# Optimization experiments

Hardware: AMD Instinct MI355X
Metric: run time of the kernel (lower is better)

## Reference

```python
import jax, jax.numpy as jnp
import numpy as np

B, N, F_IN, F_OUT = 16, 2048, 512, 512


def setup_inputs() -> dict:
    key = jax.random.key(0)
    k1, k2, k3 = jax.random.split(key, 3)
    x = jax.random.normal(k1, (B, N, F_IN), dtype=jnp.float32)
    adj = jax.random.uniform(k2, (N, N), dtype=jnp.float32)
    # Kaiming uniform fan_out: bound = sqrt(6 / fan_out)
    bound = np.sqrt(6.0 / F_OUT)
    weight = jax.random.uniform(k3, (F_IN, F_OUT), dtype=jnp.float32,
                                minval=-bound, maxval=bound)
    bias = jnp.zeros((F_OUT,), dtype=jnp.float32)
    return {"x": x, "adj": adj, "weight": weight, "bias": bias}


def reference(x, adj, weight, bias):
    # Symmetric degree normalization: D^{-1/2} A D^{-1/2}
    deg = adj.sum(axis=1)                                   # [N]
    deg_inv_sqrt = jnp.where(deg > 0, jax.lax.rsqrt(deg), 0.0)
    # row/column rescale instead of diag matmuls (same math, O(N^2))
    norm_adj = adj * deg_inv_sqrt[:, None] * deg_inv_sqrt[None, :]
    support = jnp.einsum('bni,io->bno', x, weight)          # [B,N,F_OUT]
    output = jnp.einsum('nm,bmo->bno', norm_adj, support)   # [B,N,F_OUT]
    return output + bias
```

## Files before the change

kernel.cpp:

```cpp
#include <hip/hip_runtime.h>
#include <hip/hip_bf16.h>
#include <stdint.h>

typedef __attribute__((ext_vector_type(8))) __bf16 bf16x8;
typedef __attribute__((ext_vector_type(4))) float f32x4;
typedef unsigned short u16;

__device__ __forceinline__ u16 f2bf(float f) {
  unsigned u = __builtin_bit_cast(unsigned, f);
  unsigned r = 0x7FFFu + ((u >> 16) & 1u);
  return (u16)((u + r) >> 16);
}

__device__ __forceinline__ u16 f2bf_hw(float f) {
  __hip_bfloat16 h = __float2bfloat16(f);
  return __builtin_bit_cast(u16, h);
}

__device__ __forceinline__ void gload16(const void* g, void* l) {
  __builtin_amdgcn_global_load_lds(
      (__attribute__((address_space(1))) void*)(g),
      (__attribute__((address_space(3))) void*)(l),
      16, 0, 0);
}

__global__ void row_deg_k(const float* __restrict__ adj, float* __restrict__ dis, int N) {
  int row = blockIdx.x;
  const float4* a = (const float4*)(adj + (size_t)row * N);
  float s = 0.f;
  for (int j = threadIdx.x; j < N / 4; j += 256) {
    float4 v = a[j];
    s += v.x + v.y + v.z + v.w;
  }
#pragma unroll
  for (int off = 32; off > 0; off >>= 1) s += __shfl_down(s, off, 64);
  __shared__ float wsum[4];
  if ((threadIdx.x & 63) == 0) wsum[threadIdx.x >> 6] = s;
  __syncthreads();
  if (threadIdx.x == 0) {
    float t = wsum[0] + wsum[1] + wsum[2] + wsum[3];
    dis[row] = (t > 0.f) ? (1.0f / sqrtf(t)) : 0.f;
  }
}

__global__ void conv_wt_k(const float* __restrict__ w, u16* __restrict__ wt) {
  int idx = blockIdx.x * 256 + threadIdx.x;
  int i = idx >> 9, o = idx & 511;
  wt[o * 512 + i] = f2bf(w[idx]);
}

__global__ void make_nadj_k(const float* __restrict__ adj, const float* __restrict__ dis,
                            u16* __restrict__ o, int N) {
  int idx = blockIdx.x * 256 + threadIdx.x;
  int i = idx >> 9;
  int j4 = (idx & 511) * 4;
  float di = dis[i];
  float4 a = ((const float4*)adj)[idx];
  ushort4 u;
  u.x = f2bf(a.x * di * dis[j4 + 0]);
  u.y = f2bf(a.y * di * dis[j4 + 1]);
  u.z = f2bf(a.z * di * dis[j4 + 2]);
  u.w = f2bf(a.w * di * dis[j4 + 3]);
  ((ushort4*)o)[idx] = u;
}

__launch_bounds__(512, 2)
__global__ void gemm1_xw_k(const float* __restrict__ X,
                           const u16* __restrict__ Wt,
                           u16* __restrict__ Ct, int M) {
  __shared__ __align__(16) u16 lds[65536];

  const int tid = threadIdx.x;
  const int lane = tid & 63;
  const int wid = tid >> 6;
  const int wr = wid >> 2;
  const int wc = wid & 3;

  const int flat = blockIdx.x;
  const int wg = (flat & 7) * 32 + (flat >> 3);
  const int m_t = wg >> 1;
  const int n_t = wg & 1;
  const int rowBase = m_t * 256;
  const int colBase = n_t * 256;

  const int lr = tid >> 3;
  const int kkl = (tid & 7) * 8;
  const int s = (lr & 7) << 3;
  const int kswz = kkl ^ s;
  const float* gX = X + (size_t)(rowBase + lr) * 512 + kkl;
  const u16* gB = Wt + (size_t)(colBase + lr) * 512 + kswz;
  u16* lAsw = lds + lr * 64 + kswz;
  u16* lB = lds + 32768 + lr * 64 + kkl;

  const int fr = lane & 15;
  const int rswz = (lane & 7) << 3;
  const int kp0 = ((lane >> 4) * 8) ^ rswz;
  const int kp1 = (32 | ((lane >> 4) * 8)) ^ rswz;
  const u16* fA = lds + (wr * 128 + fr) * 64;
  const u16* fB = lds + 32768 + (wc * 64 + fr) * 64;

  f32x4 acc[8][4] = {};
  f32x4 xv[4][2];

  const int NT = 8;

#define LOADX(t)                                                                     \
  _Pragma("unroll") for (int r4 = 0; r4 < 4; ++r4) {                                 \
    xv[r4][0] = *(const f32x4*)(gX + (size_t)(r4 * 64) * 512 + (t) * 64);            \
    xv[r4][1] = *(const f32x4*)(gX + (size_t)(r4 * 64) * 512 + (t) * 64 + 4);        \
  }

#define STAGE_B1(d, t)                                                               \
  _Pragma("unroll") for (int r4 = 0; r4 < 4; ++r4)                                   \
    gload16(gB + (size_t)(r4 * 64) * 512 + (size_t)(t) * 64,                         \
            lB + (d) * 16384 + r4 * 4096);

#define WRITE_A(d)                                                                   \
  _Pragma("unroll") for (int r4 = 0; r4 < 4; ++r4) {                                 \
    bf16x8 v;                                                                        \
    _Pragma("unroll") for (int i = 0; i < 4; ++i) {                                  \
      v[i] = __builtin_bit_cast(__bf16, f2bf_hw(xv[r4][0][i]));                      \
      v[4 + i] = __builtin_bit_cast(__bf16, f2bf_hw(xv[r4][1][i]));                  \
    }                                                                                \
    *(bf16x8*)(lAsw + (d) * 16384 + r4 * 4096) = v;                                  \
  }

  LOADX(0);
  STAGE_B1(0, 0);
  WRITE_A(0);
  __syncthreads();

  for (int t = 0; t < NT; ++t) {
    const int c = t & 1;
    const int cn = c ^ 1;
    const int tn = (t + 1 < NT) ? t + 1 : NT - 1;

    LOADX(tn);
    STAGE_B1(cn, tn);
    __builtin_amdgcn_sched_barrier(0);

    bf16x8 a0[8], a1[8], b0[4], b1[4];
#pragma unroll
    for (int m = 0; m < 8; ++m) {
      a0[m] = *(const bf16x8*)(fA + c * 16384 + m * 1024 + kp0);
      a1[m] = *(const bf16x8*)(fA + c * 16384 + m * 1024 + kp1);
    }
#pragma unroll
    for (int n = 0; n < 4; ++n) {
      b0[n] = *(const bf16x8*)(fB + c * 16384 + n * 1024 + kp0);
      b1[n] = *(const bf16x8*)(fB + c * 16384 + n * 1024 + kp1);
    }
#pragma unroll
    for (int m = 0; m < 8; ++m)
#pragma unroll
      for (int n = 0; n < 4; ++n)
        acc[m][n] = __builtin_amdgcn_mfma_f32_16x16x32_bf16(a0[m], b0[n], acc[m][n], 0, 0, 0);
#pragma unroll
    for (int m = 0; m < 8; ++m)
#pragma unroll
      for (int n = 0; n < 4; ++n)
        acc[m][n] = __builtin_amdgcn_mfma_f32_16x16x32_bf16(a1[m], b1[n], acc[m][n], 0, 0, 0);

    __builtin_amdgcn_sched_barrier(0);
    WRITE_A(cn);
    __syncthreads();
  }

#pragma unroll
  for (int m = 0; m < 8; ++m) {
    const int r = rowBase + wr * 128 + m * 16 + (lane >> 4) * 4;
#pragma unroll
    for (int n = 0; n < 4; ++n) {
      const int cc = colBase + wc * 64 + n * 16 + (lane & 15);
      ushort4 v;
      v.x = f2bf(acc[m][n][0]);
      v.y = f2bf(acc[m][n][1]);
      v.z = f2bf(acc[m][n][2]);
      v.w = f2bf(acc[m][n][3]);
      *reinterpret_cast<ushort4*>(&Ct[(size_t)cc * M + r]) = v;
    }
  }
#undef LOADX
#undef STAGE_B1
#undef WRITE_A
}

__launch_bounds__(512, 4)
__global__ void gemm2b_k(const u16* __restrict__ A, int lda,
                         const u16* __restrict__ Bt, int ldb,
                         float* __restrict__ C, int ldc,
                         const float* __restrict__ bias, int K,
                         int nMT, int nNT, size_t zBt, size_t zC) {
  __shared__ __align__(16) u16 lds[24576];

  const int tid = threadIdx.x;
  const int lane = tid & 63;
  const int wid = tid >> 6;
  const int wr = wid >> 2;
  const int wc = wid & 3;

  const int flat = blockIdx.x;
  const int cpx = (int)gridDim.x >> 3;
  const int wg = (flat & 7) * cpx + (flat >> 3);
  const int m_t = wg % nMT;
  const int rest = wg / nMT;
  const int n_t = rest % nNT;
  const int b = rest / nNT;
  const int rowBase = m_t * 128;
  const int colBase = n_t * 256;
  const u16* Bb = Bt + (size_t)b * zBt;

  const int lr = tid >> 3;
  const int kkl = (tid & 7) * 8;
  const int kswz = kkl ^ ((lr & 7) << 3);
  const u16* gA = A + (size_t)(rowBase + lr) * lda + kswz;
  const u16* gB = Bb + (size_t)(colBase + lr) * ldb + kswz;
  u16* lA = lds + lr * 64 + kkl;
  u16* lB = lds + 8192 + lr * 64 + kkl;

  const int fr = lane & 15;
  const int rswz = (lane & 7) << 3;
  const int kp0 = ((lane >> 4) * 8) ^ rswz;
  const int kp1 = (32 | ((lane >> 4) * 8)) ^ rswz;
  const u16* fA = lds + (wr * 64 + fr) * 64;
  const u16* fB = lds + 8192 + (wc * 64 + fr) * 64;

  f32x4 acc[4][4] = {};
  const int NT = K >> 6;

  for (int t = 0; t < NT; ++t) {
    gload16(gA + (size_t)t * 64, lA);
    gload16(gA + (size_t)64 * lda + (size_t)t * 64, lA + 4096);
#pragma unroll
    for (int r4 = 0; r4 < 4; ++r4)
      gload16(gB + (size_t)(r4 * 64) * ldb + (size_t)t * 64, lB + r4 * 4096);
    __syncthreads();

    bf16x8 a[4], bb[4];
#pragma unroll
    for (int m = 0; m < 4; ++m) a[m] = *(const bf16x8*)(fA + m * 1024 + kp0);
#pragma unroll
    for (int n = 0; n < 4; ++n) bb[n] = *(const bf16x8*)(fB + n * 1024 + kp0);
#pragma unroll
    for (int m = 0; m < 4; ++m)
#pragma unroll
      for (int n = 0; n < 4; ++n)
        acc[m][n] = __builtin_amdgcn_mfma_f32_16x16x32_bf16(a[m], bb[n], acc[m][n], 0, 0, 0);
#pragma unroll
    for (int m = 0; m < 4; ++m) a[m] = *(const bf16x8*)(fA + m * 1024 + kp1);
#pragma unroll
    for (int n = 0; n < 4; ++n) bb[n] = *(const bf16x8*)(fB + n * 1024 + kp1);
#pragma unroll
    for (int m = 0; m < 4; ++m)
#pragma unroll
      for (int n = 0; n < 4; ++n)
        acc[m][n] = __builtin_amdgcn_mfma_f32_16x16x32_bf16(a[m], bb[n], acc[m][n], 0, 0, 0);

    __syncthreads();
  }

  float* Cb = C + (size_t)b * zC;
#pragma unroll
  for (int n = 0; n < 4; ++n) {
    const int cc = colBase + wc * 64 + n * 16 + (lane & 15);
    const float bv = bias[cc];
#pragma unroll
    for (int m = 0; m < 4; ++m) {
      const int r = rowBase + wr * 64 + m * 16 + (lane >> 4) * 4;
#pragma unroll
      for (int j = 0; j < 4; ++j)
        Cb[(size_t)(r + j) * ldc + cc] = acc[m][n][j] + bv;
    }
  }
}

extern "C" void kernel_launch(void* const* d_in, const int* in_sizes, int n_in,
                              void* d_out, int out_size, void* d_ws, size_t ws_size,
                              hipStream_t stream) {
  const int B = 16, N = 2048, FIN = 512, FOUT = 512;
  const float* x    = (const float*)d_in[0];
  const float* adj  = (const float*)d_in[1];
  const float* w    = (const float*)d_in[2];
  const float* bias = (const float*)d_in[3];
  float* out = (float*)d_out;
  char* ws = (char*)d_ws;

  float* dis = (float*)ws;
  u16* wt    = (u16*)(ws + 8192);
  u16* nadj  = (u16*)(ws + 532480);
  u16* st    = (u16*)(ws + 8921088);

  row_deg_k<<<N, 256, 0, stream>>>(adj, dis, N);
  conv_wt_k<<<(FIN * FOUT) / 256, 256, 0, stream>>>(w, wt);
  make_nadj_k<<<(N * N / 4) / 256, 256, 0, stream>>>(adj, dis, nadj, N);

  gemm1_xw_k<<<dim3(256), 512, 0, stream>>>(x, wt, st, B * N);

  gemm2b_k<<<dim3(512), 512, 0, stream>>>(
      nadj, N, st, B * N, out, FOUT, bias, N, 16, 2,
      (size_t)N, (size_t)N * FOUT);
}
```

Measured before the change: 111.9 us.

## Retile both GEMMs to K=32 double-buffered LDS with smaller tiles

The first GEMM shrinks from 256x256 to 128x256 tiles, doubling the grid and allowing four blocks per CU through smaller LDS use. The second GEMM moves from a single-buffered K=64 loop with two barriers per step to a double-buffered K=32 pipeline, so global-to-LDS loads of the next slice overlap the MFMAs on the current one. Both kernels get a new swizzle for 32-wide rows. The cost is more loop iterations and barriers, and less MFMA work between them.

After: 119.1 us. 1.06x slower.

```diff
diff --git a/kernel.cpp b/kernel.cpp
--- a/kernel.cpp
+++ b/kernel.cpp
@@ -12,9 +12,9 @@
   return (u16)((u + r) >> 16);
 }
 
-__device__ __forceinline__ u16 f2bf_hw(float f) {
+__device__ __forceinline__ __bf16 f2bf_v(float f) {
   __hip_bfloat16 h = __float2bfloat16(f);
-  return __builtin_bit_cast(u16, h);
+  return __builtin_bit_cast(__bf16, h);
 }
 
 __device__ __forceinline__ void gload16(const void* g, void* l) {
@@ -64,11 +64,11 @@
   ((ushort4*)o)[idx] = u;
 }
 
-__launch_bounds__(512, 2)
-__global__ void gemm1_xw_k(const float* __restrict__ X,
-                           const u16* __restrict__ Wt,
-                           u16* __restrict__ Ct, int M) {
-  __shared__ __align__(16) u16 lds[65536];
+__launch_bounds__(512, 4)
+__global__ void gemm1b_k(const float* __restrict__ X,
+                         const u16* __restrict__ Wt,
+                         u16* __restrict__ Ct, int M) {
+  __shared__ __align__(16) u16 lds[24576];
 
   const int tid = threadIdx.x;
   const int lane = tid & 63;
@@ -77,57 +77,44 @@
   const int wc = wid & 3;
 
   const int flat = blockIdx.x;
-  const int wg = (flat & 7) * 32 + (flat >> 3);
+  const int wg = (flat & 7) * 64 + (flat >> 3);
   const int m_t = wg >> 1;
   const int n_t = wg & 1;
-  const int rowBase = m_t * 256;
+  const int rowBase = m_t * 128;
   const int colBase = n_t * 256;
 
-  const int lr = tid >> 3;
-  const int kkl = (tid & 7) * 8;
-  const int s = (lr & 7) << 3;
-  const int kswz = kkl ^ s;
-  const float* gX = X + (size_t)(rowBase + lr) * 512 + kkl;
-  const u16* gB = Wt + (size_t)(colBase + lr) * 512 + kswz;
-  u16* lAsw = lds + lr * 64 + kswz;
-  u16* lB = lds + 32768 + lr * 64 + kkl;
+  const int rowA = tid >> 2;
+  const int qA = (tid & 3) * 8;
+  const int swzA = ((rowA >> 1) & 3) << 3;
+  const float* gX = X + (size_t)(rowBase + rowA) * 512 + qA;
+  u16* lA = lds + rowA * 32 + (qA ^ swzA);
+
+  const int kkB = (tid & 3) * 8;
+  const int swzB = ((rowA >> 1) & 3) << 3;
+  const u16* gB = Wt + (size_t)(colBase + rowA) * 512 + (kkB ^ swzB);
+  u16* lBd = lds + 8192 + rowA * 32 + kkB;
 
   const int fr = lane & 15;
-  const int rswz = (lane & 7) << 3;
-  const int kp0 = ((lane >> 4) * 8) ^ rswz;
-  const int kp1 = (32 | ((lane >> 4) * 8)) ^ rswz;
-  const u16* fA = lds + (wr * 128 + fr) * 64;
-  const u16* fB = lds + 32768 + (wc * 64 + fr) * 64;
-
-  f32x4 acc[8][4] = {};
-  f32x4 xv[4][2];
-
-  const int NT = 8;
-
-#define LOADX(t)                                                                     \
-  _Pragma("unroll") for (int r4 = 0; r4 < 4; ++r4) {                                 \
-    xv[r4][0] = *(const f32x4*)(gX + (size_t)(r4 * 64) * 512 + (t) * 64);            \
-    xv[r4][1] = *(const f32x4*)(gX + (size_t)(r4 * 64) * 512 + (t) * 64 + 4);        \
-  }
-
-#define STAGE_B1(d, t)                                                               \
-  _Pragma("unroll") for (int r4 = 0; r4 < 4; ++r4)                                   \
-    gload16(gB + (size_t)(r4 * 64) * 512 + (size_t)(t) * 64,                         \
-            lB + (d) * 16384 + r4 * 4096);
-
-#define WRITE_A(d)                                                                   \
-  _Pragma("unroll") for (int r4 = 0; r4 < 4; ++r4) {                                 \
-    bf16x8 v;                                                                        \
-    _Pragma("unroll") for (int i = 0; i < 4; ++i) {                                  \
-      v[i] = __builtin_bit_cast(__bf16, f2bf_hw(xv[r4][0][i]));                      \
-      v[4 + i] = __builtin_bit_cast(__bf16, f2bf_hw(xv[r4][1][i]));                  \
-    }                                                                                \
-    *(bf16x8*)(lAsw + (d) * 16384 + r4 * 4096) = v;                                  \
-  }
-
-  LOADX(0);
-  STAGE_B1(0, 0);
-  WRITE_A(0);
+  const int rsw = ((fr >> 1) & 3) << 3;
+  const int kp = ((lane >> 4) * 8) ^ rsw;
+  const u16* fA = lds + (wr * 64 + fr) * 32;
+  const u16* fB = lds + 8192 + (wc * 64 + fr) * 32;
+
+  f32x4 acc[4][4] = {};
+  f32x4 xv0, xv1;
+
+  const int NT = 16;
+
+  xv0 = *(const f32x4*)(gX);
+  xv1 = *(const f32x4*)(gX + 4);
+  {
+    bf16x8 v;
+#pragma unroll
+    for (int i = 0; i < 4; ++i) { v[i] = f2bf_v(xv0[i]); v[4 + i] = f2bf_v(xv1[i]); }
+    *(bf16x8*)(lA) = v;
+  }
+  gload16(gB, lBd);
+  gload16(gB + (size_t)128 * 512, lBd + 4096);
   __syncthreads();
 
   for (int t = 0; t < NT; ++t) {
@@ -135,43 +122,37 @@
     const int cn = c ^ 1;
     const int tn = (t + 1 < NT) ? t + 1 : NT - 1;
 
-    LOADX(tn);
-    STAGE_B1(cn, tn);
-    __builtin_amdgcn_sched_barrier(0);
-
-    bf16x8 a0[8], a1[8], b0[4], b1[4];
-#pragma unroll
-    for (int m = 0; m < 8; ++m) {
-      a0[m] = *(const bf16x8*)(fA + c * 16384 + m * 1024 + kp0);
-      a1[m] = *(const bf16x8*)(fA + c * 16384 + m * 1024 + kp1);
+    xv0 = *(const f32x4*)(gX + tn * 32);
+    xv1 = *(const f32x4*)(gX + tn * 32 + 4);
+    gload16(gB + tn * 32, lBd + cn * 8192);
+    gload16(gB + (size_t)128 * 512 + tn * 32, lBd + cn * 8192 + 4096);
+
+    bf16x8 a[4], bb[4];
+#pragma unroll
+    for (int m = 0; m < 4; ++m) a[m] = *(const bf16x8*)(fA + c * 4096 + m * 512 + kp);
+#pragma unroll
+    for (int n = 0; n < 4; ++n) bb[n] = *(const bf16x8*)(fB + c * 8192 + n * 512 + kp);
+#pragma unroll
+    for (int m = 0; m < 4; ++m)
+#pragma unroll
+      for (int n = 0; n < 4; ++n)
+        acc[m][n] = __builtin_amdgcn_mfma_f32_16x16x32_bf16(a[m], bb[n], acc[m][n], 0, 0, 0);
+
+    {
+      bf16x8 v;
+#pragma unroll
+      for (int i = 0; i < 4; ++i) { v[i] = f2bf_v(xv0[i]); v[4 + i] = f2bf_v(xv1[i]); }
+      *(bf16x8*)(lA + cn * 4096) = v;
     }
+    __syncthreads();
+  }
+
+#pragma unroll
+  for (int m = 0; m < 4; ++m) {
+    const int r = rowBase + wr * 64 + m * 16 + (lane >> 4) * 4;
 #pragma unroll
     for (int n = 0; n < 4; ++n) {
-      b0[n] = *(const bf16x8*)(fB + c * 16384 + n * 1024 + kp0);
-      b1[n] = *(const bf16x8*)(fB + c * 16384 + n * 1024 + kp1);
-    }
-#pragma unroll
-    for (int m = 0; m < 8; ++m)
-#pragma unroll
-      for (int n = 0; n < 4; ++n)
-        acc[m][n] = __builtin_amdgcn_mfma_f32_16x16x32_bf16(a0[m], b0[n], acc[m][n], 0, 0, 0);
-#pragma unroll
-    for (int m = 0; m < 8; ++m)
-#pragma unroll
-      for (int n = 0; n < 4; ++n)
-        acc[m][n] = __builtin_amdgcn_mfma_f32_16x16x32_bf16(a1[m], b1[n], acc[m][n], 0, 0, 0);
-
-    __builtin_amdgcn_sched_barrier(0);
-    WRITE_A(cn);
-    __syncthreads();
-  }
-
-#pragma unroll
-  for (int m = 0; m < 8; ++m) {
-    const int r = rowBase + wr * 128 + m * 16 + (lane >> 4) * 4;
-#pragma unroll
-    for (int n = 0; n < 4; ++n) {
-      const int cc = colBase + wc * 64 + n * 16 + (lane & 15);
+      const int cc = colBase + wc * 64 + n * 16 + fr;
       ushort4 v;
       v.x = f2bf(acc[m][n][0]);
       v.y = f2bf(acc[m][n][1]);
@@ -180,13 +161,10 @@
       *reinterpret_cast<ushort4*>(&Ct[(size_t)cc * M + r]) = v;
     }
   }
-#undef LOADX
-#undef STAGE_B1
-#undef WRITE_A
 }
 
 __launch_bounds__(512, 4)
-__global__ void gemm2b_k(const u16* __restrict__ A, int lda,
+__global__ void gemm2c_k(const u16* __restrict__ A, int lda,
                          const u16* __restrict__ Bt, int ldb,
                          float* __restrict__ C, int ldc,
                          const float* __restrict__ bias, int K,
@@ -210,51 +188,47 @@
   const int colBase = n_t * 256;
   const u16* Bb = Bt + (size_t)b * zBt;
 
-  const int lr = tid >> 3;
-  const int kkl = (tid & 7) * 8;
-  const int kswz = kkl ^ ((lr & 7) << 3);
-  const u16* gA = A + (size_t)(rowBase + lr) * lda + kswz;
-  const u16* gB = Bb + (size_t)(colBase + lr) * ldb + kswz;
-  u16* lA = lds + lr * 64 + kkl;
-  u16* lB = lds + 8192 + lr * 64 + kkl;
+  const int rA = tid >> 2;
+  const int kk = (tid & 3) * 8;
+  const int swz = ((rA >> 1) & 3) << 3;
+  const u16* gA = A + (size_t)(rowBase + rA) * lda + (kk ^ swz);
+  const u16* gB = Bb + (size_t)(colBase + rA) * ldb + (kk ^ swz);
+  u16* lAd = lds + rA * 32 + kk;
+  u16* lBd = lds + 8192 + rA * 32 + kk;
 
   const int fr = lane & 15;
-  const int rswz = (lane & 7) << 3;
-  const int kp0 = ((lane >> 4) * 8) ^ rswz;
-  const int kp1 = (32 | ((lane >> 4) * 8)) ^ rswz;
-  const u16* fA = lds + (wr * 64 + fr) * 64;
-  const u16* fB = lds + 8192 + (wc * 64 + fr) * 64;
+  const int rsw = ((fr >> 1) & 3) << 3;
+  const int kp = ((lane >> 4) * 8) ^ rsw;
+  const u16* fA = lds + (wr * 64 + fr) * 32;
+  const u16* fB = lds + 8192 + (wc * 64 + fr) * 32;
 
   f32x4 acc[4][4] = {};
-  const int NT = K >> 6;
+  const int NT = K >> 5;
+
+  gload16(gA, lAd);
+  gload16(gB, lBd);
+  gload16(gB + (size_t)128 * ldb, lBd + 4096);
+  __syncthreads();
 
   for (int t = 0; t < NT; ++t) {
-    gload16(gA + (size_t)t * 64, lA);
-    gload16(gA + (size_t)64 * lda + (size_t)t * 64, lA + 4096);
-#pragma unroll
-    for (int r4 = 0; r4 < 4; ++r4)
-      gload16(gB + (size_t)(r4 * 64) * ldb + (size_t)t * 64, lB + r4 * 4096);
-    __syncthreads();
+    const int c = t & 1;
+    const int cn = c ^ 1;
+    const int tn = (t + 1 < NT) ? t + 1 : NT - 1;
+
+    gload16(gA + tn * 32, lAd + cn * 4096);
+    gload16(gB + tn * 32, lBd + cn * 8192);
+    gload16(gB + (size_t)128 * ldb + tn * 32, lBd + cn * 8192 + 4096);
 
     bf16x8 a[4], bb[4];
 #pragma unroll
-    for (int m = 0; m < 4; ++m) a[m] = *(const bf16x8*)(fA + m * 1024 + kp0);
-#pragma unroll
-    for (int n = 0; n < 4; ++n) bb[n] = *(const bf16x8*)(fB + n * 1024 + kp0);
+    for (int m = 0; m < 4; ++m) a[m] = *(const bf16x8*)(fA + c * 4096 + m * 512 + kp);
+#pragma unroll
+    for (int n = 0; n < 4; ++n) bb[n] = *(const bf16x8*)(fB + c * 8192 + n * 512 + kp);
 #pragma unroll
     for (int m = 0; m < 4; ++m)
 #pragma unroll
       for (int n = 0; n < 4; ++n)
         acc[m][n] = __builtin_amdgcn_mfma_f32_16x16x32_bf16(a[m], bb[n], acc[m][n], 0, 0, 0);
-#pragma unroll
-    for (int m = 0; m < 4; ++m) a[m] = *(const bf16x8*)(fA + m * 1024 + kp1);
-#pragma unroll
-    for (int n = 0; n < 4; ++n) bb[n] = *(const bf16x8*)(fB + n * 1024 + kp1);
-#pragma unroll
-    for (int m = 0; m < 4; ++m)
-#pragma unroll
-      for (int n = 0; n < 4; ++n)
-        acc[m][n] = __builtin_amdgcn_mfma_f32_16x16x32_bf16(a[m], bb[n], acc[m][n], 0, 0, 0);
 
     __syncthreads();
   }
@@ -262,7 +236,7 @@
   float* Cb = C + (size_t)b * zC;
 #pragma unroll
   for (int n = 0; n < 4; ++n) {
-    const int cc = colBase + wc * 64 + n * 16 + (lane & 15);
+    const int cc = colBase + wc * 64 + n * 16 + fr;
     const float bv = bias[cc];
 #pragma unroll
     for (int m = 0; m < 4; ++m) {
@@ -294,9 +268,9 @@
   conv_wt_k<<<(FIN * FOUT) / 256, 256, 0, stream>>>(w, wt);
   make_nadj_k<<<(N * N / 4) / 256, 256, 0, stream>>>(adj, dis, nadj, N);
 
-  gemm1_xw_k<<<dim3(256), 512, 0, stream>>>(x, wt, st, B * N);
-
-  gemm2b_k<<<dim3(512), 512, 0, stream>>>(
+  gemm1b_k<<<dim3(512), 512, 0, stream>>>(x, wt, st, B * N);
+
+  gemm2c_k<<<dim3(512), 512, 0, stream>>>(
       nadj, N, st, B * N, out, FOUT, bias, N, 16, 2,
       (size_t)N, (size_t)N * FOUT);
 }
```

## Shrink GEMM1 tile and add register-staged double-buffer pipeline to both GEMMs

Applied to the files above, without the earlier changes.

GEMM1 tiles shrink from 256 to 128 rows, so it launches 512 blocks and can fit 4 blocks per CU. GEMM2 changes from single-buffered direct-to-LDS loads with two full barriers per k-step to a software pipeline. In that pipeline the A tile is prefetched into registers and the B tile is double-buffered in LDS through async loads. Both kernels now use custom waitcnt+s_barrier sync macros, which overlap next-tile global loads with MFMA work. The risks are a single-buffered A region that relies on precise barrier placement, and a larger LDS footprint for GEMM2.

Result: slower. 124.5 us (+11.3%).

```diff
diff --git a/kernel.cpp b/kernel.cpp
--- a/kernel.cpp
+++ b/kernel.cpp
@@ -12,9 +12,9 @@
   return (u16)((u + r) >> 16);
 }
 
-__device__ __forceinline__ u16 f2bf_hw(float f) {
+__device__ __forceinline__ __bf16 f2bf_v(float f) {
   __hip_bfloat16 h = __float2bfloat16(f);
-  return __builtin_bit_cast(u16, h);
+  return __builtin_bit_cast(__bf16, h);
 }
 
 __device__ __forceinline__ void gload16(const void* g, void* l) {
@@ -23,6 +23,11 @@
       (__attribute__((address_space(3))) void*)(l),
       16, 0, 0);
 }
+
+#define SYNC_LGKM() do { asm volatile("s_waitcnt lgkmcnt(0)" ::: "memory"); \
+                         __builtin_amdgcn_s_barrier(); } while (0)
+#define SYNC_VM()   do { asm volatile("s_waitcnt vmcnt(0)" ::: "memory");   \
+                         __builtin_amdgcn_s_barrier(); } while (0)
 
 __global__ void row_deg_k(const float* __restrict__ adj, float* __restrict__ dis, int N) {
   int row = blockIdx.x;
@@ -64,11 +69,12 @@
   ((ushort4*)o)[idx] = u;
 }
 
-__launch_bounds__(512, 2)
-__global__ void gemm1_xw_k(const float* __restrict__ X,
-                           const u16* __restrict__ Wt,
-                           u16* __restrict__ Ct, int M) {
-  __shared__ __align__(16) u16 lds[65536];
+
+__launch_bounds__(512, 4)
+__global__ void gemm1d_k(const float* __restrict__ X,
+                         const u16* __restrict__ Wt,
+                         u16* __restrict__ Ct, int M) {
+  __shared__ __align__(16) u16 lds[40960];
 
   const int tid = threadIdx.x;
   const int lane = tid & 63;
@@ -77,73 +83,72 @@
   const int wc = wid & 3;
 
   const int flat = blockIdx.x;
-  const int wg = (flat & 7) * 32 + (flat >> 3);
+  const int wg = (flat & 7) * 64 + (flat >> 3);
   const int m_t = wg >> 1;
   const int n_t = wg & 1;
-  const int rowBase = m_t * 256;
+  const int rowBase = m_t * 128;
   const int colBase = n_t * 256;
 
-  const int lr = tid >> 3;
-  const int kkl = (tid & 7) * 8;
-  const int s = (lr & 7) << 3;
-  const int kswz = kkl ^ s;
-  const float* gX = X + (size_t)(rowBase + lr) * 512 + kkl;
-  const u16* gB = Wt + (size_t)(colBase + lr) * 512 + kswz;
-  u16* lAsw = lds + lr * 64 + kswz;
-  u16* lB = lds + 32768 + lr * 64 + kkl;
+  const int rA = tid >> 3;
+  const int kk = (tid & 7) * 8;
+  const int swz = (rA & 7) << 3;
+  const float* gX = X + (size_t)(rowBase + rA) * 512 + kk;
+  u16* lAw = lds + rA * 64 + (kk ^ swz);
+  const u16* gB = Wt + (size_t)(colBase + rA) * 512 + (kk ^ swz);
+  u16* lBd = lds + 8192 + rA * 64 + kk;
 
   const int fr = lane & 15;
-  const int rswz = (lane & 7) << 3;
-  const int kp0 = ((lane >> 4) * 8) ^ rswz;
-  const int kp1 = (32 | ((lane >> 4) * 8)) ^ rswz;
-  const u16* fA = lds + (wr * 128 + fr) * 64;
-  const u16* fB = lds + 32768 + (wc * 64 + fr) * 64;
-
-  f32x4 acc[8][4] = {};
-  f32x4 xv[4][2];
+  const int rsw = (lane & 7) << 3;
+  const int kp0 = ((lane >> 4) * 8) ^ rsw;
+  const int kp1 = (32 | ((lane >> 4) * 8)) ^ rsw;
+  const u16* fA = lds + (wr * 64 + fr) * 64;
+  const u16* fB = lds + 8192 + (wc * 64 + fr) * 64;
+
+  f32x4 acc[4][4] = {};
+  f32x4 xv[2][2];
 
   const int NT = 8;
 
 #define LOADX(t)                                                                     \
-  _Pragma("unroll") for (int r4 = 0; r4 < 4; ++r4) {                                 \
-    xv[r4][0] = *(const f32x4*)(gX + (size_t)(r4 * 64) * 512 + (t) * 64);            \
-    xv[r4][1] = *(const f32x4*)(gX + (size_t)(r4 * 64) * 512 + (t) * 64 + 4);        \
+  do {                                                                               \
+    xv[0][0] = *(const f32x4*)(gX + (t) * 64);                                       \
+    xv[0][1] = *(const f32x4*)(gX + (t) * 64 + 4);                                   \
+    xv[1][0] = *(const f32x4*)(gX + (size_t)64 * 512 + (t) * 64);                    \
+    xv[1][1] = *(const f32x4*)(gX + (size_t)64 * 512 + (t) * 64 + 4);                \
+  } while (0)
+
+#define WRITE_A()                                                                    \
+  _Pragma("unroll") for (int h = 0; h < 2; ++h) {                                    \
+    bf16x8 v;                                                                        \
+    _Pragma("unroll") for (int i = 0; i < 4; ++i) {                                  \
+      v[i] = f2bf_v(xv[h][0][i]); v[4 + i] = f2bf_v(xv[h][1][i]);                    \
+    }                                                                                \
+    *(bf16x8*)(lAw + h * 4096) = v;                                                  \
   }
 
 #define STAGE_B1(d, t)                                                               \
   _Pragma("unroll") for (int r4 = 0; r4 < 4; ++r4)                                   \
-    gload16(gB + (size_t)(r4 * 64) * 512 + (size_t)(t) * 64,                         \
-            lB + (d) * 16384 + r4 * 4096);
-
-#define WRITE_A(d)                                                                   \
-  _Pragma("unroll") for (int r4 = 0; r4 < 4; ++r4) {                                 \
-    bf16x8 v;                                                                        \
-    _Pragma("unroll") for (int i = 0; i < 4; ++i) {                                  \
-      v[i] = __builtin_bit_cast(__bf16, f2bf_hw(xv[r4][0][i]));                      \
-      v[4 + i] = __builtin_bit_cast(__bf16, f2bf_hw(xv[r4][1][i]));                  \
-    }                                                                                \
-    *(bf16x8*)(lAsw + (d) * 16384 + r4 * 4096) = v;                                  \
-  }
+    gload16(gB + (size_t)(r4 * 64) * 512 + (t) * 64, lBd + (d) * 16384 + r4 * 4096);
 
   LOADX(0);
   STAGE_B1(0, 0);
-  WRITE_A(0);
-  __syncthreads();
+  SYNC_VM();
 
   for (int t = 0; t < NT; ++t) {
     const int c = t & 1;
     const int cn = c ^ 1;
     const int tn = (t + 1 < NT) ? t + 1 : NT - 1;
 
+    WRITE_A();
     LOADX(tn);
     STAGE_B1(cn, tn);
-    __builtin_amdgcn_sched_barrier(0);
-
-    bf16x8 a0[8], a1[8], b0[4], b1[4];
-#pragma unroll
-    for (int m = 0; m < 8; ++m) {
-      a0[m] = *(const bf16x8*)(fA + c * 16384 + m * 1024 + kp0);
-      a1[m] = *(const bf16x8*)(fA + c * 16384 + m * 1024 + kp1);
+    SYNC_LGKM();
+
+    bf16x8 a0[4], a1[4], b0[4], b1[4];
+#pragma unroll
+    for (int m = 0; m < 4; ++m) {
+      a0[m] = *(const bf16x8*)(fA + m * 1024 + kp0);
+      a1[m] = *(const bf16x8*)(fA + m * 1024 + kp1);
     }
 #pragma unroll
     for (int n = 0; n < 4; ++n) {
@@ -151,27 +156,25 @@
       b1[n] = *(const bf16x8*)(fB + c * 16384 + n * 1024 + kp1);
     }
 #pragma unroll
-    for (int m = 0; m < 8; ++m)
+    for (int m = 0; m < 4; ++m)
 #pragma unroll
       for (int n = 0; n < 4; ++n)
         acc[m][n] = __builtin_amdgcn_mfma_f32_16x16x32_bf16(a0[m], b0[n], acc[m][n], 0, 0, 0);
 #pragma unroll
-    for (int m = 0; m < 8; ++m)
+    for (int m = 0; m < 4; ++m)
 #pragma unroll
       for (int n = 0; n < 4; ++n)
         acc[m][n] = __builtin_amdgcn_mfma_f32_16x16x32_bf16(a1[m], b1[n], acc[m][n], 0, 0, 0);
 
-    __builtin_amdgcn_sched_barrier(0);
-    WRITE_A(cn);
-    __syncthreads();
-  }
-
-#pragma unroll
-  for (int m = 0; m < 8; ++m) {
-    const int r = rowBase + wr * 128 + m * 16 + (lane >> 4) * 4;
+    SYNC_VM();
+  }
+
+#pragma unroll
+  for (int m = 0; m < 4; ++m) {
+    const int r = rowBase + wr * 64 + m * 16 + (lane >> 4) * 4;
 #pragma unroll
     for (int n = 0; n < 4; ++n) {
-      const int cc = colBase + wc * 64 + n * 16 + (lane & 15);
+      const int cc = colBase + wc * 64 + n * 16 + fr;
       ushort4 v;
       v.x = f2bf(acc[m][n][0]);
       v.y = f2bf(acc[m][n][1]);
@@ -181,17 +184,17 @@
     }
   }
 #undef LOADX
+#undef WRITE_A
 #undef STAGE_B1
-#undef WRITE_A
 }
 
 __launch_bounds__(512, 4)
-__global__ void gemm2b_k(const u16* __restrict__ A, int lda,
+__global__ void gemm2d_k(const u16* __restrict__ A, int lda,
                          const u16* __restrict__ Bt, int ldb,
                          float* __restrict__ C, int ldc,
                          const float* __restrict__ bias, int K,
                          int nMT, int nNT, size_t zBt, size_t zC) {
-  __shared__ __align__(16) u16 lds[24576];
+  __shared__ __align__(16) u16 lds[40960];
 
   const int tid = threadIdx.x;
   const int lane = tid & 63;
@@ -210,59 +213,82 @@
   const int colBase = n_t * 256;
   const u16* Bb = Bt + (size_t)b * zBt;
 
-  const int lr = tid >> 3;
-  const int kkl = (tid & 7) * 8;
-  const int kswz = kkl ^ ((lr & 7) << 3);
-  const u16* gA = A + (size_t)(rowBase + lr) * lda + kswz;
-  const u16* gB = Bb + (size_t)(colBase + lr) * ldb + kswz;
-  u16* lA = lds + lr * 64 + kkl;
-  u16* lB = lds + 8192 + lr * 64 + kkl;
+  const int rA = tid >> 3;
+  const int kk = (tid & 7) * 8;
+  const int swz = (rA & 7) << 3;
+  const u16* gA = A + (size_t)(rowBase + rA) * lda + kk;
+  u16* lAw = lds + rA * 64 + (kk ^ swz);
+  const u16* gB = Bb + (size_t)(colBase + rA) * ldb + (kk ^ swz);
+  u16* lBd = lds + 8192 + rA * 64 + kk;
 
   const int fr = lane & 15;
-  const int rswz = (lane & 7) << 3;
-  const int kp0 = ((lane >> 4) * 8) ^ rswz;
-  const int kp1 = (32 | ((lane >> 4) * 8)) ^ rswz;
+  const int rsw = (lane & 7) << 3;
+  const int kp0 = ((lane >> 4) * 8) ^ rsw;
+  const int kp1 = (32 | ((lane >> 4) * 8)) ^ rsw;
   const u16* fA = lds + (wr * 64 + fr) * 64;
   const u16* fB = lds + 8192 + (wc * 64 + fr) * 64;
 
   f32x4 acc[4][4] = {};
+  bf16x8 aR[2];
+
   const int NT = K >> 6;
 
+#define LOADA(t)                                                                     \
+  do {                                                                               \
+    aR[0] = *(const bf16x8*)(gA + (t) * 64);                                         \
+    aR[1] = *(const bf16x8*)(gA + (size_t)64 * lda + (t) * 64);                      \
+  } while (0)
+
+#define WRITE_A()                                                                    \
+  do { *(bf16x8*)(lAw) = aR[0]; *(bf16x8*)(lAw + 4096) = aR[1]; } while (0)
+
+#define STAGE_B1(d, t)                                                               \
+  _Pragma("unroll") for (int r4 = 0; r4 < 4; ++r4)                                   \
+    gload16(gB + (size_t)(r4 * 64) * ldb + (t) * 64, lBd + (d) * 16384 + r4 * 4096);
+
+  LOADA(0);
+  STAGE_B1(0, 0);
+  SYNC_VM();
+
   for (int t = 0; t < NT; ++t) {
-    gload16(gA + (size_t)t * 64, lA);
-    gload16(gA + (size_t)64 * lda + (size_t)t * 64, lA + 4096);
-#pragma unroll
-    for (int r4 = 0; r4 < 4; ++r4)
-      gload16(gB + (size_t)(r4 * 64) * ldb + (size_t)t * 64, lB + r4 * 4096);
-    __syncthreads();
-
-    bf16x8 a[4], bb[4];
-#pragma unroll
-    for (int m = 0; m < 4; ++m) a[m] = *(const bf16x8*)(fA + m * 1024 + kp0);
-#pragma unroll
-    for (int n = 0; n < 4; ++n) bb[n] = *(const bf16x8*)(fB + n * 1024 + kp0);
+    const int c = t & 1;
+    const int cn = c ^ 1;
+    const int tn = (t + 1 < NT) ? t + 1 : NT - 1;
+
+    WRITE_A();
+    LOADA(tn);
+    STAGE_B1(cn, tn);
+    SYNC_LGKM();
+
+    bf16x8 a0[4], a1[4], b0[4], b1[4];
+#pragma unroll
+    for (int m = 0; m < 4; ++m) {
+      a0[m] = *(const bf16x8*)(fA + m * 1024 + kp0);
+      a1[m] = *(const bf16x8*)(fA + m * 1024 + kp1);
+    }
+#pragma unroll
+    for (int n = 0; n < 4; ++n) {
+      b0[n] = *(const bf16x8*)(fB + c * 16384 + n * 1024 + kp0);
+      b1[n] = *(const bf16x8*)(fB + c * 16384 + n * 1024 + kp1);
+    }
 #pragma unroll
     for (int m = 0; m < 4; ++m)
 #pragma unroll
       for (int n = 0; n < 4; ++n)
-        acc[m][n] = __builtin_amdgcn_mfma_f32_16x16x32_bf16(a[m], bb[n], acc[m][n], 0, 0, 0);
-#pragma unroll
-    for (int m = 0; m < 4; ++m) a[m] = *(const bf16x8*)(fA + m * 1024 + kp1);
-#pragma unroll
-    for (int n = 0; n < 4; ++n) bb[n] = *(const bf16x8*)(fB + n * 1024 + kp1);
+        acc[m][n] = __builtin_amdgcn_mfma_f32_16x16x32_bf16(a0[m], b0[n], acc[m][n], 0, 0, 0);
 #pragma unroll
     for (int m = 0; m < 4; ++m)
 #pragma unroll
       for (int n = 0; n < 4; ++n)
-        acc[m][n] = __builtin_amdgcn_mfma_f32_16x16x32_bf16(a[m], bb[n], acc[m][n], 0, 0, 0);
-
-    __syncthreads();
+        acc[m][n] = __builtin_amdgcn_mfma_f32_16x16x32_bf16(a1[m], b1[n], acc[m][n], 0, 0, 0);
+
+    SYNC_VM();
   }
 
   float* Cb = C + (size_t)b * zC;
 #pragma unroll
   for (int n = 0; n < 4; ++n) {
-    const int cc = colBase + wc * 64 + n * 16 + (lane & 15);
+    const int cc = colBase + wc * 64 + n * 16 + fr;
     const float bv = bias[cc];
 #pragma unroll
     for (int m = 0; m < 4; ++m) {
@@ -272,6 +298,9 @@
         Cb[(size_t)(r + j) * ldc + cc] = acc[m][n][j] + bv;
     }
   }
+#undef LOADA
+#undef WRITE_A
+#undef STAGE_B1
 }
 
 extern "C" void kernel_launch(void* const* d_in, const int* in_sizes, int n_in,
@@ -294,9 +323,9 @@
   conv_wt_k<<<(FIN * FOUT) / 256, 256, 0, stream>>>(w, wt);
   make_nadj_k<<<(N * N / 4) / 256, 256, 0, stream>>>(adj, dis, nadj, N);
 
-  gemm1_xw_k<<<dim3(256), 512, 0, stream>>>(x, wt, st, B * N);
-
-  gemm2b_k<<<dim3(512), 512, 0, stream>>>(
+  gemm1d_k<<<dim3(512), 512, 0, stream>>>(x, wt, st, B * N);
+
+  gemm2d_k<<<dim3(512), 512, 0, stream>>>(
       nadj, N, st, B * N, out, FOUT, bias, N, 16, 2,
       (size_t)N, (size_t)N * FOUT);
 }
```

## Shrink X·W GEMM tile to 128x256, single-buffer LDS, raise occupancy

Applied to the files above, without the earlier changes.

The first GEMM now uses 128-row tiles instead of 256, with a single LDS buffer (48KB instead of 128KB) and launch bounds allowing 4 blocks per CU. The grid doubles to 512 blocks so all CUs get work at higher occupancy. The double-buffered software pipeline is replaced by a load/sync/compute/sync loop that relies on occupancy to hide latency. This trades per-block data reuse and intra-block overlap for more concurrent waves.

Measured after the change: 114.7 us. 2.5% more time.

```diff
diff --git a/kernel.cpp b/kernel.cpp
--- a/kernel.cpp
+++ b/kernel.cpp
@@ -12,9 +12,9 @@
   return (u16)((u + r) >> 16);
 }
 
-__device__ __forceinline__ u16 f2bf_hw(float f) {
+__device__ __forceinline__ __bf16 f2bf_v(float f) {
   __hip_bfloat16 h = __float2bfloat16(f);
-  return __builtin_bit_cast(u16, h);
+  return __builtin_bit_cast(__bf16, h);
 }
 
 __device__ __forceinline__ void gload16(const void* g, void* l) {
@@ -64,11 +64,11 @@
   ((ushort4*)o)[idx] = u;
 }
 
-__launch_bounds__(512, 2)
-__global__ void gemm1_xw_k(const float* __restrict__ X,
-                           const u16* __restrict__ Wt,
-                           u16* __restrict__ Ct, int M) {
-  __shared__ __align__(16) u16 lds[65536];
+__launch_bounds__(512, 4)
+__global__ void gemm1e_k(const float* __restrict__ X,
+                         const u16* __restrict__ Wt,
+                         u16* __restrict__ Ct, int M) {
+  __shared__ __align__(16) u16 lds[24576];
 
   const int tid = threadIdx.x;
   const int lane = tid & 63;
@@ -77,101 +77,95 @@
   const int wc = wid & 3;
 
   const int flat = blockIdx.x;
-  const int wg = (flat & 7) * 32 + (flat >> 3);
+  const int wg = (flat & 7) * 64 + (flat >> 3);
   const int m_t = wg >> 1;
   const int n_t = wg & 1;
-  const int rowBase = m_t * 256;
+  const int rowBase = m_t * 128;
   const int colBase = n_t * 256;
 
-  const int lr = tid >> 3;
-  const int kkl = (tid & 7) * 8;
-  const int s = (lr & 7) << 3;
-  const int kswz = kkl ^ s;
-  const float* gX = X + (size_t)(rowBase + lr) * 512 + kkl;
-  const u16* gB = Wt + (size_t)(colBase + lr) * 512 + kswz;
-  u16* lAsw = lds + lr * 64 + kswz;
-  u16* lB = lds + 32768 + lr * 64 + kkl;
+  const int rA = tid >> 3;
+  const int kk = (tid & 7) * 8;
+  const int swz = (rA & 7) << 3;
+  const float* gX = X + (size_t)(rowBase + rA) * 512 + kk;
+  u16* lAw = lds + rA * 64 + (kk ^ swz);
+  const u16* gB = Wt + (size_t)(colBase + rA) * 512 + (kk ^ swz);
+  u16* lBd = lds + 8192 + rA * 64 + kk;
 
   const int fr = lane & 15;
-  const int rswz = (lane & 7) << 3;
-  const int kp0 = ((lane >> 4) * 8) ^ rswz;
-  const int kp1 = (32 | ((lane >> 4) * 8)) ^ rswz;
-  const u16* fA = lds + (wr * 128 + fr) * 64;
-  const u16* fB = lds + 32768 + (wc * 64 + fr) * 64;
-
-  f32x4 acc[8][4] = {};
-  f32x4 xv[4][2];
+  const int rsw = (lane & 7) << 3;
+  const int kp0 = ((lane >> 4) * 8) ^ rsw;
+  const int kp1 = (32 | ((lane >> 4) * 8)) ^ rsw;
+  const u16* fA = lds + (wr * 64 + fr) * 64;
+  const u16* fB = lds + 8192 + (wc * 64 + fr) * 64;
+
+  f32x4 acc[4][4] = {};
+  f32x4 xv[2][2];
 
   const int NT = 8;
 
 #define LOADX(t)                                                                     \
-  _Pragma("unroll") for (int r4 = 0; r4 < 4; ++r4) {                                 \
-    xv[r4][0] = *(const f32x4*)(gX + (size_t)(r4 * 64) * 512 + (t) * 64);            \
-    xv[r4][1] = *(const f32x4*)(gX + (size_t)(r4 * 64) * 512 + (t) * 64 + 4);        \
-  }
-
-#define STAGE_B1(d, t)                                                               \
-  _Pragma("unroll") for (int r4 = 0; r4 < 4; ++r4)                                   \
-    gload16(gB + (size_t)(r4 * 64) * 512 + (size_t)(t) * 64,                         \
-            lB + (d) * 16384 + r4 * 4096);
-
-#define WRITE_A(d)                                                                   \
-  _Pragma("unroll") for (int r4 = 0; r4 < 4; ++r4) {                                 \
+  do {                                                                               \
+    xv[0][0] = *(const f32x4*)(gX + (t) * 64);                                       \
+    xv[0][1] = *(const f32x4*)(gX + (t) * 64 + 4);                                   \
+    xv[1][0] = *(const f32x4*)(gX + (size_t)64 * 512 + (t) * 64);                    \
+    xv[1][1] = *(const f32x4*)(gX + (size_t)64 * 512 + (t) * 64 + 4);                \
+  } while (0)
+
+#define WRITE_A()                                                                    \
+  _Pragma("unroll") for (int h = 0; h < 2; ++h) {                                    \
     bf16x8 v;                                                                        \
     _Pragma("unroll") for (int i = 0; i < 4; ++i) {                                  \
-      v[i] = __builtin_bit_cast(__bf16, f2bf_hw(xv[r4][0][i]));                      \
-      v[4 + i] = __builtin_bit_cast(__bf16, f2bf_hw(xv[r4][1][i]));                  \
+      v[i] = f2bf_v(xv[h][0][i]); v[4 + i] = f2bf_v(xv[h][1][i]);                    \
     }                                                                                \
-    *(bf16x8*)(lAsw + (d) * 16384 + r4 * 4096) = v;                                  \
-  }
+    *(bf16x8*)(lAw + h * 4096) = v;                                                  \
+  }
+
+#define STAGE_B1(t)                                                                  \
+  _Pragma("unroll") for (int r4 = 0; r4 < 4; ++r4)                                   \
+    gload16(gB + (size_t)(r4 * 64) * 512 + (t) * 64, lBd + r4 * 4096);
 
   LOADX(0);
-  STAGE_B1(0, 0);
-  WRITE_A(0);
-  __syncthreads();
 
   for (int t = 0; t < NT; ++t) {
-    const int c = t & 1;
-    const int cn = c ^ 1;
     const int tn = (t + 1 < NT) ? t + 1 : NT - 1;
 
+    STAGE_B1(t);
+    WRITE_A();
+    __syncthreads();
+
     LOADX(tn);
-    STAGE_B1(cn, tn);
-    __builtin_amdgcn_sched_barrier(0);
-
-    bf16x8 a0[8], a1[8], b0[4], b1[4];
-#pragma unroll
-    for (int m = 0; m < 8; ++m) {
-      a0[m] = *(const bf16x8*)(fA + c * 16384 + m * 1024 + kp0);
-      a1[m] = *(const bf16x8*)(fA + c * 16384 + m * 1024 + kp1);
+
+    bf16x8 a0[4], a1[4], b0[4], b1[4];
+#pragma unroll
+    for (int m = 0; m < 4; ++m) {
+      a0[m] = *(const bf16x8*)(fA + m * 1024 + kp0);
+      a1[m] = *(const bf16x8*)(fA + m * 1024 + kp1);
     }
 #pragma unroll
     for (int n = 0; n < 4; ++n) {
-      b0[n] = *(const bf16x8*)(fB + c * 16384 + n * 1024 + kp0);
-      b1[n] = *(const bf16x8*)(fB + c * 16384 + n * 1024 + kp1);
-    }
-#pragma unroll
-    for (int m = 0; m < 8; ++m)
+      b0[n] = *(const bf16x8*)(fB + n * 1024 + kp0);
+      b1[n] = *(const bf16x8*)(fB + n * 1024 + kp1);
+    }
+#pragma unroll
+    for (int m = 0; m < 4; ++m)
 #pragma unroll
       for (int n = 0; n < 4; ++n)
         acc[m][n] = __builtin_amdgcn_mfma_f32_16x16x32_bf16(a0[m], b0[n], acc[m][n], 0, 0, 0);
 #pragma unroll
-    for (int m = 0; m < 8; ++m)
+    for (int m = 0; m < 4; ++m)
 #pragma unroll
       for (int n = 0; n < 4; ++n)
         acc[m][n] = __builtin_amdgcn_mfma_f32_16x16x32_bf16(a1[m], b1[n], acc[m][n], 0, 0, 0);
 
-    __builtin_amdgcn_sched_barrier(0);
-    WRITE_A(cn);
-    __syncthreads();
-  }
-
-#pragma unroll
-  for (int m = 0; m < 8; ++m) {
-    const int r = rowBase + wr * 128 + m * 16 + (lane >> 4) * 4;
+    __syncthreads();
+  }
+
+#pragma unroll
+  for (int m = 0; m < 4; ++m) {
+    const int r = rowBase + wr * 64 + m * 16 + (lane >> 4) * 4;
 #pragma unroll
     for (int n = 0; n < 4; ++n) {
-      const int cc = colBase + wc * 64 + n * 16 + (lane & 15);
+      const int cc = colBase + wc * 64 + n * 16 + fr;
       ushort4 v;
       v.x = f2bf(acc[m][n][0]);
       v.y = f2bf(acc[m][n][1]);
@@ -181,8 +175,8 @@
     }
   }
 #undef LOADX
+#undef WRITE_A
 #undef STAGE_B1
-#undef WRITE_A
 }
 
 __launch_bounds__(512, 4)
@@ -262,7 +256,7 @@
   float* Cb = C + (size_t)b * zC;
 #pragma unroll
   for (int n = 0; n < 4; ++n) {
-    const int cc = colBase + wc * 64 + n * 16 + (lane & 15);
+    const int cc = colBase + wc * 64 + n * 16 + fr;
     const float bv = bias[cc];
 #pragma unroll
     for (int m = 0; m < 4; ++m) {
@@ -294,7 +288,7 @@
   conv_wt_k<<<(FIN * FOUT) / 256, 256, 0, stream>>>(w, wt);
   make_nadj_k<<<(N * N / 4) / 256, 256, 0, stream>>>(adj, dis, nadj, N);
 
-  gemm1_xw_k<<<dim3(256), 512, 0, stream>>>(x, wt, st, B * N);
+  gemm1e_k<<<dim3(512), 512, 0, stream>>>(x, wt, st, B * N);
 
   gemm2b_k<<<dim3(512), 512, 0, stream>>>(
       nadj, N, st, B * N, out, FOUT, bias, N, 16, 2,
```
